# Kernel tuning notes

Measured on AMD Instinct MI355X. Metric: run time of the kernel, lower is better.

The kernel has to match this reference:

```python
import jax, jax.numpy as jnp
import numpy as np

B, U, D, N, O = 128, 16, 256, 1024, 256
RES_CONN, IN_CONN, BIAS_P = 0.2, 0.2, 0.5


def _fixed_bernoulli(rng, heads, rows, cols, conn):
    # each column has exactly nb = int(conn*rows) ones (as in the torch code)
    nb = max(1, int(conn * rows))
    r = rng.random((heads, rows, cols))
    thr = np.sort(r, axis=1)[:, nb - 1:nb, :]
    return (r <= thr).astype(np.float32)


def setup_inputs() -> dict:
    rng = np.random.default_rng(0)
    # recurrent weights: normal * fixed-bernoulli mask, normalized by spectral radius
    W = rng.normal(size=(U, N, N)).astype(np.float32) * _fixed_bernoulli(rng, U, N, N, RES_CONN)
    sr0 = np.abs(np.linalg.eigvals(W.astype(np.float64))).max(axis=-1).astype(np.float32).reshape(U, 1, 1)
    W = W / sr0
    Win = _fixed_bernoulli(rng, U, D, N, IN_CONN)
    bias = (rng.random((U, 1, N)) < BIAS_P).astype(np.float32)
    Wout = rng.normal(size=(U, N, O)).astype(np.float32)
    adaptive_lr = rng.random((U, D, 1)).astype(np.float32)
    sr = rng.random((U, 1, 1)).astype(np.float32)
    temperature = np.ones((1,), np.float32)
    X = rng.normal(size=(B, U, D)).astype(np.float32)
    state = rng.normal(size=(B, U, N)).astype(np.float32)
    arrs = dict(X=X, state=state, W=W, Win=Win, bias=bias, Wout=Wout,
                sr=sr, adaptive_lr=adaptive_lr, temperature=temperature)
    return {k: jnp.asarray(v) for k, v in arrs.items()}


def reference(X, state, W, Win, bias, Wout, sr, adaptive_lr, temperature):
    # X: [B,U,D] -> [B,U,1,D]; state: [B,U,N] -> [B,U,1,N]
    x = X[:, :, None, :]
    s = state[:, :, None, :]
    # adaptive per-unit learning rate: softmax over the units axis
    lr = jax.nn.softmax(jnp.einsum('buid,udk->buik', x, adaptive_lr) / temperature, axis=1)  # [B,U,1,1]
    feed = jnp.einsum('buid,udn->buin', x, Win)            # [B,U,1,N]
    echo = jnp.einsum('buin,unm->buim', s, W * sr) + bias  # [B,U,1,N]
    new_state = (1.0 - lr) * s + lr * jnp.tanh(feed + echo)
    output = jnp.einsum('buin,uno->buio', new_state, Wout)  # [B,U,1,O]
    return new_state[:, :, 0, :], output[:, :, 0, :]
```

## Files before the change

### kernel.cpp

```cpp
#include <hip/hip_runtime.h>
#include <math.h>

#define Bsz 128
#define Usz 16
#define Dsz 256
#define Nsz 1024
#define Osz 256
#define BK  64
#define LDT 72

typedef __attribute__((ext_vector_type(2))) unsigned int u32x2;
typedef __attribute__((ext_vector_type(4))) unsigned int u32x4;
typedef __attribute__((ext_vector_type(4))) float f32x4;
typedef __attribute__((ext_vector_type(8))) short bf16x8;

__device__ __forceinline__ unsigned int fbits(float f) {
    union { float f; unsigned int u; } v; v.f = f; return v.u;
}
__device__ __forceinline__ unsigned int pk(float lo, float hi) {
    return __builtin_amdgcn_perm(fbits(hi), fbits(lo), 0x07060302u);
}
__device__ __forceinline__ unsigned short bf16t(float f) {
    return (unsigned short)(fbits(f) >> 16);
}

__device__ __forceinline__ void sync_nodrain() {
    __builtin_amdgcn_sched_barrier(0);
    asm volatile("s_waitcnt lgkmcnt(0)");
    __builtin_amdgcn_sched_barrier(0);
    __builtin_amdgcn_s_barrier();
    __builtin_amdgcn_sched_barrier(0);
}

__global__ __launch_bounds__(256)
void lr_kernel(const float* __restrict__ X, const float* __restrict__ alr,
               const float* __restrict__ temp, float* __restrict__ lr)
{
    const int b = blockIdx.x;
    const int t = threadIdx.x;
    const int u = t >> 4;
    const int l = t & 15;
    const f32x4* xp = (const f32x4*)(X + ((size_t)b * Usz + u) * Dsz + l * 16);
    const f32x4* ap = (const f32x4*)(alr + (size_t)u * Dsz + l * 16);
    float s = 0.f;
    #pragma unroll
    for (int j = 0; j < 4; j++) {
        const f32x4 xv = xp[j], av = ap[j];
        s += xv[0]*av[0] + xv[1]*av[1] + xv[2]*av[2] + xv[3]*av[3];
    }
    s += __shfl_down(s, 8, 16);
    s += __shfl_down(s, 4, 16);
    s += __shfl_down(s, 2, 16);
    s += __shfl_down(s, 1, 16);
    __shared__ float logits[16];
    if (l == 0) logits[u] = s;
    __syncthreads();
    if (t < 16) {
        const float T = temp[0];
        float m = -1e30f;
        #pragma unroll
        for (int i = 0; i < 16; i++) m = fmaxf(m, logits[i] / T);
        float sum = 0.f;
        #pragma unroll
        for (int i = 0; i < 16; i++) sum += expf(logits[i] / T - m);
        lr[(size_t)b * Usz + t] = expf(logits[t] / T - m) / sum;
    }
}

__global__ __launch_bounds__(512)
void state_gemm(const float* __restrict__ X, const float* __restrict__ state,
                const float* __restrict__ W, const float* __restrict__ Win,
                const float* __restrict__ bias, const float* __restrict__ sr,
                const float* __restrict__ lr, float* __restrict__ out0)
{
    const int id = blockIdx.x;
    const int u  = id & 15;
    const int nt = id >> 4;

    const int tid  = threadIdx.x;
    const int wave = tid >> 6;
    const int lane = tid & 63;
    const int l16  = lane & 15, kgl = lane >> 4;
    const int wm = wave & 3, wn = wave >> 2;

    __shared__ unsigned short As[2][128 * LDT];
    __shared__ unsigned short Bs[2][32 * LDT];

    const float sru = sr[u];
    const int col0 = nt * 32;

    const int rA = tid >> 2;
    const int cA = (tid & 3) * 16;
    const int kB = tid >> 3;
    const int nB = (tid & 7) * 4;
    const int gB = kB >> 3, kL = kB & 7;

    f32x4 rAE[4], rAO[4];
    f32x4 rBE,    rBO;

    auto ldA = [&](int s, f32x4 (&ra)[4]) {
        const int k0 = s * BK;
        const float* base = (k0 < Dsz)
            ? X     + ((size_t)rA * Usz + u) * Dsz + k0 + cA
            : state + ((size_t)rA * Usz + u) * Nsz + (k0 - Dsz) + cA;
        #pragma unroll
        for (int j = 0; j < 4; j++) ra[j] = *(const f32x4*)(base + 4 * j);
    };
    auto ldB = [&](int s, f32x4& rb) {
        const int k0 = s * BK;
        const float* base = (k0 < Dsz)
            ? Win + (size_t)u * Dsz * Nsz + (size_t)(k0 + kB) * Nsz + col0 + nB
            : W   + (size_t)u * Nsz * Nsz + (size_t)(k0 - Dsz + kB) * Nsz + col0 + nB;
        rb = *(const f32x4*)base;
    };
    auto wrA = [&](int p, f32x4 (&ra)[4]) {
        u32x4 w0, w1;
        w0[0] = pk(ra[0][0], ra[0][1]); w0[1] = pk(ra[0][2], ra[0][3]);
        w0[2] = pk(ra[1][0], ra[1][1]); w0[3] = pk(ra[1][2], ra[1][3]);
        w1[0] = pk(ra[2][0], ra[2][1]); w1[1] = pk(ra[2][2], ra[2][3]);
        w1[2] = pk(ra[3][0], ra[3][1]); w1[3] = pk(ra[3][2], ra[3][3]);
        *(u32x4*)&As[p][rA * LDT + cA]     = w0;
        *(u32x4*)&As[p][rA * LDT + cA + 8] = w1;
    };
    auto wrB = [&](int p, f32x4& rb, float sc) {
        const int c = tid & 7;
        const int go = ((gB ^ c) << 3) + kL;
        #pragma unroll
        for (int e = 0; e < 4; e++)
            Bs[p][(nB + e) * LDT + go] = bf16t(rb[e] * sc);
    };
    auto rdB = [&](int p, int kk) -> bf16x8 {
        const int n = wn * 16 + l16;
        const int go = (((kk * 4 + kgl) ^ (n >> 2)) << 3);
        return *(const bf16x8*)&Bs[p][n * LDT + go];
    };

    f32x4 acc[2] = {};
    auto comp = [&](int p) {
        #pragma unroll
        for (int kk = 0; kk < 2; kk++) {
            const bf16x8 bf = rdB(p, kk);
            #pragma unroll
            for (int mi = 0; mi < 2; mi++) {
                const bf16x8 af = *(const bf16x8*)&As[p][(wm * 32 + mi * 16 + l16) * LDT + kk * 32 + kgl * 8];
                acc[mi] = __builtin_amdgcn_mfma_f32_16x16x32_bf16(af, bf, acc[mi], 0, 0, 0);
            }
        }
    };
    auto scB = [&](int s) -> float { return (s * BK < Dsz) ? 1.f : sru; };

    ldA(0, rAE); ldB(0, rBE);
    ldA(1, rAO); ldB(1, rBO);
    wrA(0, rAE); wrB(0, rBE, scB(0));
    sync_nodrain();

    for (int s2 = 0; s2 < 10; s2++) {
        const int s = 2 * s2;
        if (s + 2 < 20) { ldA(s + 2, rAE); ldB(s + 2, rBE); }
        wrA(1, rAO); wrB(1, rBO, scB(s + 1));
        comp(0);
        sync_nodrain();
        if (s + 3 < 20) { ldA(s + 3, rAO); ldB(s + 3, rBO); }
        if (s + 2 < 20) { wrA(0, rAE); wrB(0, rBE, scB(s + 2)); }
        comp(1);
        sync_nodrain();
    }

    const int gcol = col0 + wn * 16 + l16;
    const float bi = bias[u * Nsz + gcol];
    #pragma unroll
    for (int mi = 0; mi < 2; mi++) {
        #pragma unroll
        for (int rg = 0; rg < 4; rg++) {
            const int grow = wm * 32 + mi * 16 + kgl * 4 + rg;
            const size_t idx = ((size_t)grow * Usz + u) * Nsz + gcol;
            const float th = tanhf(acc[mi][rg] + bi);
            const float lv = lr[grow * Usz + u];
            out0[idx] = (1.f - lv) * state[idx] + lv * th;
        }
    }
}

__global__ __launch_bounds__(512)
void out_gemm(const float* __restrict__ ns, const float* __restrict__ Wout,
              float* __restrict__ dst, int nsteps, int partial)
{
    const int id = blockIdx.x;
    const int ot = id & 7;
    const int u  = (id >> 3) & 15;
    const int ks = id >> 7;
    const int kbase = ks * nsteps * BK;

    const int tid  = threadIdx.x;
    const int wave = tid >> 6;
    const int lane = tid & 63;
    const int l16  = lane & 15, kgl = lane >> 4;
    const int wm = wave & 3, wn = wave >> 2;

    __shared__ unsigned short As[2][128 * LDT];
    __shared__ unsigned short Bs[2][32 * LDT];

    const int col0 = ot * 32;
    const int rA = tid >> 2;
    const int cA = (tid & 3) * 16;
    const int kB = tid >> 3;
    const int nB = (tid & 7) * 4;
    const int gB = kB >> 3, kL = kB & 7;

    f32x4 rAE[4], rAO[4];
    f32x4 rBE,    rBO;

    auto ldA = [&](int s, f32x4 (&ra)[4]) {
        const float* base = ns + ((size_t)rA * Usz + u) * Nsz + kbase + s * BK + cA;
        #pragma unroll
        for (int j = 0; j < 4; j++) ra[j] = *(const f32x4*)(base + 4 * j);
    };
    auto ldB = [&](int s, f32x4& rb) {
        rb = *(const f32x4*)(Wout + (size_t)u * Nsz * Osz
                             + (size_t)(kbase + s * BK + kB) * Osz + col0 + nB);
    };
    auto wrA = [&](int p, f32x4 (&ra)[4]) {
        u32x4 w0, w1;
        w0[0] = pk(ra[0][0], ra[0][1]); w0[1] = pk(ra[0][2], ra[0][3]);
        w0[2] = pk(ra[1][0], ra[1][1]); w0[3] = pk(ra[1][2], ra[1][3]);
        w1[0] = pk(ra[2][0], ra[2][1]); w1[1] = pk(ra[2][2], ra[2][3]);
        w1[2] = pk(ra[3][0], ra[3][1]); w1[3] = pk(ra[3][2], ra[3][3]);
        *(u32x4*)&As[p][rA * LDT + cA]     = w0;
        *(u32x4*)&As[p][rA * LDT + cA + 8] = w1;
    };
    auto wrB = [&](int p, f32x4& rb) {
        const int c = tid & 7;
        const int go = ((gB ^ c) << 3) + kL;
        #pragma unroll
        for (int e = 0; e < 4; e++)
            Bs[p][(nB + e) * LDT + go] = bf16t(rb[e]);
    };
    auto rdB = [&](int p, int kk) -> bf16x8 {
        const int n = wn * 16 + l16;
        const int go = (((kk * 4 + kgl) ^ (n >> 2)) << 3);
        return *(const bf16x8*)&Bs[p][n * LDT + go];
    };

    f32x4 acc[2] = {};
    auto comp = [&](int p) {
        #pragma unroll
        for (int kk = 0; kk < 2; kk++) {
            const bf16x8 bf = rdB(p, kk);
            #pragma unroll
            for (int mi = 0; mi < 2; mi++) {
                const bf16x8 af = *(const bf16x8*)&As[p][(wm * 32 + mi * 16 + l16) * LDT + kk * 32 + kgl * 8];
                acc[mi] = __builtin_amdgcn_mfma_f32_16x16x32_bf16(af, bf, acc[mi], 0, 0, 0);
            }
        }
    };

    ldA(0, rAE); ldB(0, rBE);
    ldA(1, rAO); ldB(1, rBO);
    wrA(0, rAE); wrB(0, rBE);
    sync_nodrain();

    for (int s2 = 0; s2 < nsteps / 2; s2++) {
        const int s = 2 * s2;
        if (s + 2 < nsteps) { ldA(s + 2, rAE); ldB(s + 2, rBE); }
        wrA(1, rAO); wrB(1, rBO);
        comp(0);
        sync_nodrain();
        if (s + 3 < nsteps) { ldA(s + 3, rAO); ldB(s + 3, rBO); }
        if (s + 2 < nsteps) { wrA(0, rAE); wrB(0, rBE); }
        comp(1);
        sync_nodrain();
    }

    const int gcol = col0 + wn * 16 + l16;
    #pragma unroll
    for (int mi = 0; mi < 2; mi++) {
        #pragma unroll
        for (int rg = 0; rg < 4; rg++) {
            const int grow = wm * 32 + mi * 16 + kgl * 4 + rg;
            if (partial)
                dst[(((size_t)ks * 16 + u) * 128 + grow) * 256 + gcol] = acc[mi][rg];
            else
                dst[((size_t)grow * Usz + u) * Osz + gcol] = acc[mi][rg];
        }
    }
}

__global__ __launch_bounds__(256)
void out_reduce(const float* __restrict__ part, float* __restrict__ out1)
{
    const size_t i = (size_t)blockIdx.x * 256 + threadIdx.x;
    const size_t base = i * 4;
    const int m = (int)(base >> 12);
    const int u = (int)((base >> 8) & 15);
    const int o = (int)(base & 255);

    const size_t pb = ((size_t)u * 128 + m) * 256 + o;
    const size_t slab = (size_t)16 * 128 * 256;
    f32x4 s = *(const f32x4*)(part + pb);
    s += *(const f32x4*)(part + pb + slab);
    s += *(const f32x4*)(part + pb + 2 * slab);
    s += *(const f32x4*)(part + pb + 3 * slab);
    *(f32x4*)(out1 + base) = s;
}

extern "C" void kernel_launch(void* const* d_in, const int* in_sizes, int n_in,
                              void* d_out, int out_size, void* d_ws, size_t ws_size,
                              hipStream_t stream)
{
    (void)in_sizes; (void)n_in; (void)out_size;
    const float* X     = (const float*)d_in[0];
    const float* state = (const float*)d_in[1];
    const float* W     = (const float*)d_in[2];
    const float* Win   = (const float*)d_in[3];
    const float* bias  = (const float*)d_in[4];
    const float* Wout  = (const float*)d_in[5];
    const float* sr    = (const float*)d_in[6];
    const float* alr   = (const float*)d_in[7];
    const float* temp  = (const float*)d_in[8];

    float* out0 = (float*)d_out;
    float* out1 = out0 + (size_t)Bsz * Usz * Nsz;
    float* lr   = (float*)d_ws;

    const size_t p_off   = 8192;
    const size_t p_bytes = (size_t)4 * 16 * 128 * 256 * 4;

    lr_kernel<<<Bsz, 256, 0, stream>>>(X, alr, temp, lr);
    state_gemm<<<512, 512, 0, stream>>>(X, state, W, Win, bias, sr, lr, out0);

    if (ws_size >= p_off + p_bytes) {
        float* part = (float*)((char*)d_ws + p_off);
        out_gemm<<<512, 512, 0, stream>>>(out0, Wout, part, 4, 1);
        out_reduce<<<512, 256, 0, stream>>>(part, out1);
    } else {
        out_gemm<<<128, 512, 0, stream>>>(out0, Wout, out1, 16, 0);
    }
}
```

Measured before the change: 185.5 us.

## Pre-pack operands to bf16 MFMA fragment layout and run register-only GEMMs

Adds packing kernels that convert W·sr, Win, Wout, X/state and the new state into bf16 tiles already laid out as MFMA fragments. New GEMM kernels then load these fragments straight into registers with a 3-stage register prefetch and skip the LDS staging. The point is to remove shared-memory traffic, barriers and per-tile conversion from the GEMMs. In exchange it adds several extra launches and a full rewrite of the weights every call, about 40 MB of bf16 written and read again, and it only runs when the workspace is large enough.

```diff
diff --git a/kernel.cpp b/kernel.cpp
--- a/kernel.cpp
+++ b/kernel.cpp
@@ -67,11 +67,222 @@
     }
 }
 
+
+__global__ __launch_bounds__(256)
+void pack_A(const float* __restrict__ X, const float* __restrict__ state,
+            unsigned short* __restrict__ Abf)
+{
+    const int t = blockIdx.x * 256 + threadIdx.x;
+    const int kq = t % 160;
+    const int mu = t / 160;
+    const int u = mu & 15, m = mu >> 4;
+    const float* sp = (kq < 32)
+        ? X     + (size_t)mu * Dsz + kq * 8
+        : state + (size_t)mu * Nsz + (kq - 32) * 8;
+    const f32x4 v0 = *(const f32x4*)sp;
+    const f32x4 v1 = *(const f32x4*)(sp + 4);
+    u32x4 w;
+    w[0]=pk(v0[0],v0[1]); w[1]=pk(v0[2],v0[3]); w[2]=pk(v1[0],v1[1]); w[3]=pk(v1[2],v1[3]);
+    *(u32x4*)(Abf + (size_t)(u*8 + (m>>4))*20480 + (kq>>2)*512 + (kq&3)*128 + (m&15)*8) = w;
+}
+
+__global__ __launch_bounds__(256)
+void pack_ns(const float* __restrict__ ns, unsigned short* __restrict__ NsP)
+{
+    const int t = blockIdx.x * 256 + threadIdx.x;
+    const int kq = t & 127;
+    const int mu = t >> 7;
+    const int u = mu & 15, m = mu >> 4;
+    const float* sp = ns + (size_t)mu * Nsz + kq * 8;
+    const f32x4 v0 = *(const f32x4*)sp;
+    const f32x4 v1 = *(const f32x4*)(sp + 4);
+    u32x4 w;
+    w[0]=pk(v0[0],v0[1]); w[1]=pk(v0[2],v0[3]); w[2]=pk(v1[0],v1[1]); w[3]=pk(v1[2],v1[3]);
+    *(u32x4*)(NsP + (size_t)(u*8 + (m>>4))*16384 + (kq>>2)*512 + (kq&3)*128 + (m&15)*8) = w;
+}
+
+__global__ __launch_bounds__(256)
+void prep_w(const float* __restrict__ srcA, const float* __restrict__ srcB,
+            const float* __restrict__ scale, unsigned short* __restrict__ dst,
+            int KA, int Ktot, int N, int S, int Tn)
+{
+    const int nblkN = N >> 6;
+    const int per_u = (Ktot >> 6) * nblkN;
+    const int bid = blockIdx.x;
+    const int u   = bid / per_u;
+    const int rem = bid % per_u;
+    const int kt  = rem / nblkN;
+    const int nt4 = rem % nblkN;
+
+    const int t  = threadIdx.x;
+    const int kr = t >> 4;
+    const int nc = (t & 15) * 4;
+    const int n0 = nt4 * 64;
+
+    const float sc = scale ? scale[u] : 1.f;
+
+    __shared__ float tl[64][68];
+
+    #pragma unroll
+    for (int r = 0; r < 4; r++) {
+        const int kl = kr + r * 16;
+        const int k  = kt * 64 + kl;
+        const float* sp = (k < KA)
+            ? srcA + ((size_t)u * KA + k) * N + n0 + nc
+            : srcB + ((size_t)u * (Ktot - KA) + (k - KA)) * N + n0 + nc;
+        f32x4 v = *(const f32x4*)sp;
+        if (k >= KA) v *= sc;
+        *(f32x4*)&tl[kl][nc] = v;
+    }
+    __syncthreads();
+    #pragma unroll
+    for (int fi = 0; fi < 2; fi++) {
+        const int f   = t + fi * 256;
+        const int l   = f & 15;
+        const int g   = (f >> 4) & 7;
+        const int ntl = f >> 7;
+        float x[8];
+        #pragma unroll
+        for (int i = 0; i < 8; i++) x[i] = tl[g*8 + i][ntl*16 + l];
+        u32x4 w;
+        w[0]=pk(x[0],x[1]); w[1]=pk(x[2],x[3]); w[2]=pk(x[4],x[5]); w[3]=pk(x[6],x[7]);
+        const int tn = nt4*4 + ntl;
+        const int s  = kt*2 + (g>>2);
+        *(u32x4*)(dst + ((size_t)(u*Tn + tn)*S + s)*512 + (g&3)*128 + l*8) = w;
+    }
+}
+
+__global__ __launch_bounds__(512, 4)
+void state_gemm_reg(const float* __restrict__ state,
+                    const unsigned short* __restrict__ Abf,
+                    const unsigned short* __restrict__ Bp,
+                    const float* __restrict__ bias, const float* __restrict__ lr,
+                    float* __restrict__ out0)
+{
+    const int id  = blockIdx.x;
+    const int u   = id & 15;
+    const int nt2 = id >> 4;
+
+    const int tid = threadIdx.x;
+    const int wave = tid >> 6, lane = tid & 63;
+    const int l16 = lane & 15, kgl = lane >> 4;
+    const int wm = wave & 3, wn = wave >> 2;
+    const int mt0 = wm * 2;
+    const int tn  = nt2 * 2 + wn;
+
+    const unsigned short* pa0 = Abf + (size_t)(u*8 + mt0)    *20480 + kgl*128 + l16*8;
+    const unsigned short* pa1 = Abf + (size_t)(u*8 + mt0 + 1)*20480 + kgl*128 + l16*8;
+    const unsigned short* pb  = Bp  + (size_t)(u*64 + tn)    *20480 + kgl*128 + l16*8;
+
+    bf16x8 a0[3], a1[3], bb[3];
+    f32x4 acc0 = {}, acc1 = {};
+
+    a0[0] = *(const bf16x8*)(pa0);        a1[0] = *(const bf16x8*)(pa1);        bb[0] = *(const bf16x8*)(pb);
+    a0[1] = *(const bf16x8*)(pa0 + 512);  a1[1] = *(const bf16x8*)(pa1 + 512);  bb[1] = *(const bf16x8*)(pb + 512);
+
+    #pragma unroll
+    for (int s = 0; s < 40; s++) {
+        const int st = s % 3, nx = (s + 2) % 3;
+        if (s + 2 < 40) {
+            a0[nx] = *(const bf16x8*)(pa0 + (size_t)(s + 2) * 512);
+            a1[nx] = *(const bf16x8*)(pa1 + (size_t)(s + 2) * 512);
+            bb[nx] = *(const bf16x8*)(pb  + (size_t)(s + 2) * 512);
+        }
+        acc0 = __builtin_amdgcn_mfma_f32_16x16x32_bf16(a0[st], bb[st], acc0, 0, 0, 0);
+        acc1 = __builtin_amdgcn_mfma_f32_16x16x32_bf16(a1[st], bb[st], acc1, 0, 0, 0);
+    }
+
+    const int gcol = tn * 16 + l16;
+    const float bi = bias[u * Nsz + gcol];
+    #pragma unroll
+    for (int mi = 0; mi < 2; mi++) {
+        const f32x4 a = mi ? acc1 : acc0;
+        #pragma unroll
+        for (int rg = 0; rg < 4; rg++) {
+            const int grow = (mt0 + mi) * 16 + kgl * 4 + rg;
+            const size_t idx = ((size_t)grow * Usz + u) * Nsz + gcol;
+            const float th = tanhf(a[rg] + bi);
+            const float lv = lr[grow * Usz + u];
+            out0[idx] = (1.f - lv) * state[idx] + lv * th;
+        }
+    }
+}
+
+__global__ __launch_bounds__(512, 4)
+void out_gemm_reg(const unsigned short* __restrict__ NsP,
+                  const unsigned short* __restrict__ Wp,
+                  float* __restrict__ part)
+{
+    const int id = blockIdx.x;
+    const int ot = id & 7;
+    const int u  = (id >> 3) & 15;
+    const int ks = id >> 7;
+    const int sb = ks * 8;
+
+    const int tid = threadIdx.x;
+    const int wave = tid >> 6, lane = tid & 63;
+    const int l16 = lane & 15, kgl = lane >> 4;
+    const int wm = wave & 3, wn = wave >> 2;
+    const int mt0 = wm * 2;
+    const int tn  = ot * 2 + wn;
+
+    const unsigned short* pa0 = NsP + (size_t)(u*8 + mt0)    *16384 + (size_t)sb*512 + kgl*128 + l16*8;
+    const unsigned short* pa1 = NsP + (size_t)(u*8 + mt0 + 1)*16384 + (size_t)sb*512 + kgl*128 + l16*8;
+    const unsigned short* pb  = Wp  + (size_t)(u*16 + tn)    *16384 + (size_t)sb*512 + kgl*128 + l16*8;
+
+    bf16x8 a0[3], a1[3], bb[3];
+    f32x4 acc0 = {}, acc1 = {};
+
+    a0[0] = *(const bf16x8*)(pa0);        a1[0] = *(const bf16x8*)(pa1);        bb[0] = *(const bf16x8*)(pb);
+    a0[1] = *(const bf16x8*)(pa0 + 512);  a1[1] = *(const bf16x8*)(pa1 + 512);  bb[1] = *(const bf16x8*)(pb + 512);
+
+    #pragma unroll
+    for (int s = 0; s < 8; s++) {
+        const int st = s % 3, nx = (s + 2) % 3;
+        if (s + 2 < 8) {
+            a0[nx] = *(const bf16x8*)(pa0 + (size_t)(s + 2) * 512);
+            a1[nx] = *(const bf16x8*)(pa1 + (size_t)(s + 2) * 512);
+            bb[nx] = *(const bf16x8*)(pb  + (size_t)(s + 2) * 512);
+        }
+        acc0 = __builtin_amdgcn_mfma_f32_16x16x32_bf16(a0[st], bb[st], acc0, 0, 0, 0);
+        acc1 = __builtin_amdgcn_mfma_f32_16x16x32_bf16(a1[st], bb[st], acc1, 0, 0, 0);
+    }
+
+    const int gcol = tn * 16 + l16;
+    #pragma unroll
+    for (int mi = 0; mi < 2; mi++) {
+        const f32x4 a = mi ? acc1 : acc0;
+        #pragma unroll
+        for (int rg = 0; rg < 4; rg++) {
+            const int grow = (mt0 + mi) * 16 + kgl * 4 + rg;
+            part[(((size_t)ks * 16 + u) * 128 + grow) * 256 + gcol] = a[rg];
+        }
+    }
+}
+
+__global__ __launch_bounds__(256)
+void out_reduce(const float* __restrict__ part, float* __restrict__ out1)
+{
+    const size_t i = (size_t)blockIdx.x * 256 + threadIdx.x;
+    const size_t base = i * 4;
+    const int m = (int)(base >> 12);
+    const int u = (int)((base >> 8) & 15);
+    const int o = (int)(base & 255);
+
+    const size_t pb = ((size_t)u * 128 + m) * 256 + o;
+    const size_t slab = (size_t)16 * 128 * 256;
+    f32x4 s = *(const f32x4*)(part + pb);
+    s += *(const f32x4*)(part + pb + slab);
+    s += *(const f32x4*)(part + pb + 2 * slab);
+    s += *(const f32x4*)(part + pb + 3 * slab);
+    *(f32x4*)(out1 + base) = s;
+}
+
 __global__ __launch_bounds__(512)
-void state_gemm(const float* __restrict__ X, const float* __restrict__ state,
-                const float* __restrict__ W, const float* __restrict__ Win,
-                const float* __restrict__ bias, const float* __restrict__ sr,
-                const float* __restrict__ lr, float* __restrict__ out0)
+void state_gemm_fb(const float* __restrict__ X, const float* __restrict__ state,
+                   const float* __restrict__ W, const float* __restrict__ Win,
+                   const float* __restrict__ bias, const float* __restrict__ sr,
+                   const float* __restrict__ lr, float* __restrict__ out0)
 {
     const int id = blockIdx.x;
     const int u  = id & 15;
@@ -182,8 +393,8 @@
 }
 
 __global__ __launch_bounds__(512)
-void out_gemm(const float* __restrict__ ns, const float* __restrict__ Wout,
-              float* __restrict__ dst, int nsteps, int partial)
+void out_gemm_fb(const float* __restrict__ ns, const float* __restrict__ Wout,
+                 float* __restrict__ dst, int nsteps, int partial)
 {
     const int id = blockIdx.x;
     const int ot = id & 7;
@@ -285,24 +496,6 @@
     }
 }
 
-__global__ __launch_bounds__(256)
-void out_reduce(const float* __restrict__ part, float* __restrict__ out1)
-{
-    const size_t i = (size_t)blockIdx.x * 256 + threadIdx.x;
-    const size_t base = i * 4;
-    const int m = (int)(base >> 12);
-    const int u = (int)((base >> 8) & 15);
-    const int o = (int)(base & 255);
-
-    const size_t pb = ((size_t)u * 128 + m) * 256 + o;
-    const size_t slab = (size_t)16 * 128 * 256;
-    f32x4 s = *(const f32x4*)(part + pb);
-    s += *(const f32x4*)(part + pb + slab);
-    s += *(const f32x4*)(part + pb + 2 * slab);
-    s += *(const f32x4*)(part + pb + 3 * slab);
-    *(f32x4*)(out1 + base) = s;
-}
-
 extern "C" void kernel_launch(void* const* d_in, const int* in_sizes, int n_in,
                               void* d_out, int out_size, void* d_ws, size_t ws_size,
                               hipStream_t stream)
@@ -322,17 +515,41 @@
     float* out1 = out0 + (size_t)Bsz * Usz * Nsz;
     float* lr   = (float*)d_ws;
 
-    const size_t p_off   = 8192;
-    const size_t p_bytes = (size_t)4 * 16 * 128 * 256 * 4;
+    const size_t p_off    = 8192;
+    const size_t p_bytes  = (size_t)4 * 16 * 128 * 256 * 4;
+    const size_t bp_off   = p_off + p_bytes;
+    const size_t bp_bytes = (size_t)16 * 1280 * 1024 * 2;
+    const size_t wo_off   = bp_off + bp_bytes;
+    const size_t wo_bytes = (size_t)16 * 1024 * 256 * 2;
+    const size_t ab_off   = wo_off + wo_bytes;
+    const size_t ab_bytes = (size_t)128 * 16 * 1280 * 2;
+    const size_t ns_off   = ab_off + ab_bytes;
+    const size_t ns_bytes = (size_t)128 * 16 * 1024 * 2;
+    const size_t need     = ns_off + ns_bytes;
 
     lr_kernel<<<Bsz, 256, 0, stream>>>(X, alr, temp, lr);
-    state_gemm<<<512, 512, 0, stream>>>(X, state, W, Win, bias, sr, lr, out0);
-
-    if (ws_size >= p_off + p_bytes) {
+
+    if (ws_size >= need) {
+        float*          part = (float*)((char*)d_ws + p_off);
+        unsigned short* Bp   = (unsigned short*)((char*)d_ws + bp_off);
+        unsigned short* Wp   = (unsigned short*)((char*)d_ws + wo_off);
+        unsigned short* Abf  = (unsigned short*)((char*)d_ws + ab_off);
+        unsigned short* NsP  = (unsigned short*)((char*)d_ws + ns_off);
+
+        prep_w<<<5120, 256, 0, stream>>>(Win, W, sr, Bp, Dsz, 1280, Nsz, 40, 64);
+        prep_w<<<1024, 256, 0, stream>>>(Wout, Wout, nullptr, Wp, Nsz, Nsz, Osz, 32, 16);
+        pack_A<<<1280, 256, 0, stream>>>(X, state, Abf);
+        state_gemm_reg<<<512, 512, 0, stream>>>(state, Abf, Bp, bias, lr, out0);
+        pack_ns<<<1024, 256, 0, stream>>>(out0, NsP);
+        out_gemm_reg<<<512, 512, 0, stream>>>(NsP, Wp, part);
+        out_reduce<<<512, 256, 0, stream>>>(part, out1);
+    } else if (ws_size >= p_off + p_bytes) {
         float* part = (float*)((char*)d_ws + p_off);
-        out_gemm<<<512, 512, 0, stream>>>(out0, Wout, part, 4, 1);
+        state_gemm_fb<<<512, 512, 0, stream>>>(X, state, W, Win, bias, sr, lr, out0);
+        out_gemm_fb<<<512, 512, 0, stream>>>(out0, Wout, part, 4, 1);
         out_reduce<<<512, 256, 0, stream>>>(part, out1);
     } else {
-        out_gemm<<<128, 512, 0, stream>>>(out0, Wout, out1, 16, 0);
-    }
-}
+        state_gemm_fb<<<512, 512, 0, stream>>>(X, state, W, Win, bias, sr, lr, out0);
+        out_gemm_fb<<<128, 512, 0, stream>>>(out0, Wout, out1, 16, 0);
+    }
+}
```

Result: slower. 204.0 us (+9.9%).

## Split-K the state GEMM into two halves with a separate tanh epilogue kernel

Applied to the files above, without the earlier changes.

The state GEMM (K=1280, from X plus state) is split into two K halves of 640. That doubles the grid to 1024 blocks for better occupancy on the many CUs. Partial sums go to workspace, and a new elementwise kernel reduces them and applies bias, tanh and the lr blend. The split kernel also switches its A tile in LDS to an XOR-swizzled unpadded layout instead of padded rows. The cost is extra global traffic for the partials (16 MB written then read) and one more kernel launch.

```diff
diff --git a/kernel.cpp b/kernel.cpp
--- a/kernel.cpp
+++ b/kernel.cpp
@@ -67,15 +67,16 @@
     }
 }
 
-__global__ __launch_bounds__(512)
-void state_gemm(const float* __restrict__ X, const float* __restrict__ state,
-                const float* __restrict__ W, const float* __restrict__ Win,
-                const float* __restrict__ bias, const float* __restrict__ sr,
-                const float* __restrict__ lr, float* __restrict__ out0)
+__global__ __launch_bounds__(512, 8)
+void state_gemm_sk(const float* __restrict__ X, const float* __restrict__ state,
+                   const float* __restrict__ W, const float* __restrict__ Win,
+                   const float* __restrict__ sr, float* __restrict__ part2)
 {
     const int id = blockIdx.x;
     const int u  = id & 15;
-    const int nt = id >> 4;
+    const int nt = (id >> 4) & 31;
+    const int ks = id >> 9;
+    const int kbase = ks * 640;
 
     const int tid  = threadIdx.x;
     const int wave = tid >> 6;
@@ -83,12 +84,148 @@
     const int l16  = lane & 15, kgl = lane >> 4;
     const int wm = wave & 3, wn = wave >> 2;
 
+    __shared__ unsigned short As[2][128 * 64];
+    __shared__ unsigned short Bs[2][32 * 64];
+
+    const float sru = sr[u];
+    const int col0 = nt * 32;
+
+    const int rA = tid >> 2;
+    const int cA = (tid & 3) * 16;
+    const int g0 = (tid & 3) * 2;
+    const int sw = rA & 7;
+    const int kB = tid >> 3;
+    const int nB = (tid & 7) * 4;
+    const int gB = kB >> 3, kL = kB & 7;
+
+    f32x4 rAE[4], rAO[4];
+    f32x4 rBE,    rBO;
+
+    auto ldA = [&](int s, f32x4 (&ra)[4]) {
+        const int k0 = kbase + s * BK;
+        const float* base = (k0 < Dsz)
+            ? X     + ((size_t)rA * Usz + u) * Dsz + k0 + cA
+            : state + ((size_t)rA * Usz + u) * Nsz + (k0 - Dsz) + cA;
+        #pragma unroll
+        for (int j = 0; j < 4; j++) ra[j] = *(const f32x4*)(base + 4 * j);
+    };
+    auto ldB = [&](int s, f32x4& rb) {
+        const int k0 = kbase + s * BK;
+        const float* base = (k0 < Dsz)
+            ? Win + (size_t)u * Dsz * Nsz + (size_t)(k0 + kB) * Nsz + col0 + nB
+            : W   + (size_t)u * Nsz * Nsz + (size_t)(k0 - Dsz + kB) * Nsz + col0 + nB;
+        rb = *(const f32x4*)base;
+    };
+    auto wrA = [&](int p, f32x4 (&ra)[4]) {
+        u32x4 w0, w1;
+        w0[0] = pk(ra[0][0], ra[0][1]); w0[1] = pk(ra[0][2], ra[0][3]);
+        w0[2] = pk(ra[1][0], ra[1][1]); w0[3] = pk(ra[1][2], ra[1][3]);
+        w1[0] = pk(ra[2][0], ra[2][1]); w1[1] = pk(ra[2][2], ra[2][3]);
+        w1[2] = pk(ra[3][0], ra[3][1]); w1[3] = pk(ra[3][2], ra[3][3]);
+        *(u32x4*)&As[p][rA * 64 + ((g0       ^ sw) << 3)] = w0;
+        *(u32x4*)&As[p][rA * 64 + (((g0 | 1) ^ sw) << 3)] = w1;
+    };
+    auto wrB = [&](int p, f32x4& rb, float sc) {
+        const int c = tid & 7;
+        const int go = ((gB ^ c) << 3) + kL;
+        #pragma unroll
+        for (int e = 0; e < 4; e++)
+            Bs[p][(nB + e) * 64 + go] = bf16t(rb[e] * sc);
+    };
+    auto rdB = [&](int p, int kk) -> bf16x8 {
+        const int n = wn * 16 + l16;
+        const int go = (((kk * 4 + kgl) ^ (n >> 2)) << 3);
+        return *(const bf16x8*)&Bs[p][n * 64 + go];
+    };
+
+    f32x4 acc[2] = {};
+    auto comp = [&](int p) {
+        #pragma unroll
+        for (int kk = 0; kk < 2; kk++) {
+            const bf16x8 bf = rdB(p, kk);
+            #pragma unroll
+            for (int mi = 0; mi < 2; mi++) {
+                const int r = wm * 32 + mi * 16 + l16;
+                const bf16x8 af = *(const bf16x8*)&As[p][r * 64 + (((kk * 4 + kgl) ^ (r & 7)) << 3)];
+                acc[mi] = __builtin_amdgcn_mfma_f32_16x16x32_bf16(af, bf, acc[mi], 0, 0, 0);
+            }
+        }
+    };
+    auto scB = [&](int s) -> float { return (kbase + s * BK < Dsz) ? 1.f : sru; };
+
+    ldA(0, rAE); ldB(0, rBE);
+    ldA(1, rAO); ldB(1, rBO);
+    wrA(0, rAE); wrB(0, rBE, scB(0));
+    sync_nodrain();
+
+    for (int s2 = 0; s2 < 5; s2++) {
+        const int s = 2 * s2;
+        if (s + 2 < 10) { ldA(s + 2, rAE); ldB(s + 2, rBE); }
+        wrA(1, rAO); wrB(1, rBO, scB(s + 1));
+        comp(0);
+        sync_nodrain();
+        if (s + 3 < 10) { ldA(s + 3, rAO); ldB(s + 3, rBO); }
+        if (s + 2 < 10) { wrA(0, rAE); wrB(0, rBE, scB(s + 2)); }
+        comp(1);
+        sync_nodrain();
+    }
+
+    const int gcol = col0 + wn * 16 + l16;
+    float* dst = part2 + (size_t)ks * 128 * Usz * Nsz;
+    #pragma unroll
+    for (int mi = 0; mi < 2; mi++) {
+        #pragma unroll
+        for (int rg = 0; rg < 4; rg++) {
+            const int grow = wm * 32 + mi * 16 + kgl * 4 + rg;
+            dst[((size_t)grow * Usz + u) * Nsz + gcol] = acc[mi][rg];
+        }
+    }
+}
+
+__global__ __launch_bounds__(256)
+void state_ep(const float* __restrict__ part2, const float* __restrict__ state,
+              const float* __restrict__ bias, const float* __restrict__ lr,
+              float* __restrict__ out0)
+{
+    const size_t i = (size_t)blockIdx.x * 256 + threadIdx.x;
+    const size_t base = i * 4;
+    const int m = (int)(i >> 12);
+    const int u = (int)((i >> 8) & 15);
+    const int n = (int)((i & 255) * 4);
+
+    const size_t slab = (size_t)128 * Usz * Nsz;
+    f32x4 s = *(const f32x4*)(part2 + base);
+    s += *(const f32x4*)(part2 + base + slab);
+    const f32x4 bi = *(const f32x4*)(bias + u * Nsz + n);
+    const f32x4 st = *(const f32x4*)(state + base);
+    const float lv = lr[m * Usz + u];
+    f32x4 o;
+    #pragma unroll
+    for (int e = 0; e < 4; e++)
+        o[e] = (1.f - lv) * st[e] + lv * tanhf(s[e] + bi[e]);
+    *(f32x4*)(out0 + base) = o;
+}
+
+__global__ __launch_bounds__(512)
+void out_gemm_fb(const float* __restrict__ ns, const float* __restrict__ Wout,
+                 float* __restrict__ dst, int nsteps, int partial)
+{
+    const int id = blockIdx.x;
+    const int ot = id & 7;
+    const int u  = (id >> 3) & 15;
+    const int ks = id >> 7;
+    const int kbase = ks * nsteps * BK;
+
+    const int tid  = threadIdx.x;
+    const int wave = tid >> 6;
+    const int lane = tid & 63;
+    const int l16  = lane & 15, kgl = lane >> 4;
+    const int wm = wave & 3, wn = wave >> 2;
+
     __shared__ unsigned short As[2][128 * LDT];
     __shared__ unsigned short Bs[2][32 * LDT];
 
-    const float sru = sr[u];
-    const int col0 = nt * 32;
-
+    const int col0 = ot * 32;
     const int rA = tid >> 2;
     const int cA = (tid & 3) * 16;
     const int kB = tid >> 3;
@@ -99,19 +236,13 @@
     f32x4 rBE,    rBO;
 
     auto ldA = [&](int s, f32x4 (&ra)[4]) {
-        const int k0 = s * BK;
-        const float* base = (k0 < Dsz)
-            ? X     + ((size_t)rA * Usz + u) * Dsz + k0 + cA
-            : state + ((size_t)rA * Usz + u) * Nsz + (k0 - Dsz) + cA;
+        const float* base = ns + ((size_t)rA * Usz + u) * Nsz + kbase + s * BK + cA;
         #pragma unroll
         for (int j = 0; j < 4; j++) ra[j] = *(const f32x4*)(base + 4 * j);
     };
     auto ldB = [&](int s, f32x4& rb) {
-        const int k0 = s * BK;
-        const float* base = (k0 < Dsz)
-            ? Win + (size_t)u * Dsz * Nsz + (size_t)(k0 + kB) * Nsz + col0 + nB
-            : W   + (size_t)u * Nsz * Nsz + (size_t)(k0 - Dsz + kB) * Nsz + col0 + nB;
-        rb = *(const f32x4*)base;
+        rb = *(const f32x4*)(Wout + (size_t)u * Nsz * Osz
+                             + (size_t)(kbase + s * BK + kB) * Osz + col0 + nB);
     };
     auto wrA = [&](int p, f32x4 (&ra)[4]) {
         u32x4 w0, w1;
@@ -122,12 +253,12 @@
         *(u32x4*)&As[p][rA * LDT + cA]     = w0;
         *(u32x4*)&As[p][rA * LDT + cA + 8] = w1;
     };
-    auto wrB = [&](int p, f32x4& rb, float sc) {
+    auto wrB = [&](int p, f32x4& rb) {
         const int c = tid & 7;
         const int go = ((gB ^ c) << 3) + kL;
         #pragma unroll
         for (int e = 0; e < 4; e++)
-            Bs[p][(nB + e) * LDT + go] = bf16t(rb[e] * sc);
+            Bs[p][(nB + e) * LDT + go] = bf16t(rb[e]);
     };
     auto rdB = [&](int p, int kk) -> bf16x8 {
         const int n = wn * 16 + l16;
@@ -147,49 +278,65 @@
             }
         }
     };
-    auto scB = [&](int s) -> float { return (s * BK < Dsz) ? 1.f : sru; };
 
     ldA(0, rAE); ldB(0, rBE);
     ldA(1, rAO); ldB(1, rBO);
-    wrA(0, rAE); wrB(0, rBE, scB(0));
+    wrA(0, rAE); wrB(0, rBE);
     sync_nodrain();
 
-    for (int s2 = 0; s2 < 10; s2++) {
+    for (int s2 = 0; s2 < nsteps / 2; s2++) {
         const int s = 2 * s2;
-        if (s + 2 < 20) { ldA(s + 2, rAE); ldB(s + 2, rBE); }
-        wrA(1, rAO); wrB(1, rBO, scB(s + 1));
+        if (s + 2 < nsteps) { ldA(s + 2, rAE); ldB(s + 2, rBE); }
+        wrA(1, rAO); wrB(1, rBO);
         comp(0);
         sync_nodrain();
-        if (s + 3 < 20) { ldA(s + 3, rAO); ldB(s + 3, rBO); }
-        if (s + 2 < 20) { wrA(0, rAE); wrB(0, rBE, scB(s + 2)); }
+        if (s + 3 < nsteps) { ldA(s + 3, rAO); ldB(s + 3, rBO); }
+        if (s + 2 < nsteps) { wrA(0, rAE); wrB(0, rBE); }
         comp(1);
         sync_nodrain();
     }
 
     const int gcol = col0 + wn * 16 + l16;
-    const float bi = bias[u * Nsz + gcol];
     #pragma unroll
     for (int mi = 0; mi < 2; mi++) {
         #pragma unroll
         for (int rg = 0; rg < 4; rg++) {
             const int grow = wm * 32 + mi * 16 + kgl * 4 + rg;
-            const size_t idx = ((size_t)grow * Usz + u) * Nsz + gcol;
-            const float th = tanhf(acc[mi][rg] + bi);
-            const float lv = lr[grow * Usz + u];
-            out0[idx] = (1.f - lv) * state[idx] + lv * th;
-        }
-    }
+            if (partial)
+                dst[(((size_t)ks * 16 + u) * 128 + grow) * 256 + gcol] = acc[mi][rg];
+            else
+                dst[((size_t)grow * Usz + u) * Osz + gcol] = acc[mi][rg];
+        }
+    }
+}
+
+__global__ __launch_bounds__(256)
+void out_reduce(const float* __restrict__ part, float* __restrict__ out1)
+{
+    const size_t i = (size_t)blockIdx.x * 256 + threadIdx.x;
+    const size_t base = i * 4;
+    const int m = (int)(base >> 12);
+    const int u = (int)((base >> 8) & 15);
+    const int o = (int)(base & 255);
+
+    const size_t pb = ((size_t)u * 128 + m) * 256 + o;
+    const size_t slab = (size_t)16 * 128 * 256;
+    f32x4 s = *(const f32x4*)(part + pb);
+    s += *(const f32x4*)(part + pb + slab);
+    s += *(const f32x4*)(part + pb + 2 * slab);
+    s += *(const f32x4*)(part + pb + 3 * slab);
+    *(f32x4*)(out1 + base) = s;
 }
 
 __global__ __launch_bounds__(512)
-void out_gemm(const float* __restrict__ ns, const float* __restrict__ Wout,
-              float* __restrict__ dst, int nsteps, int partial)
+void state_gemm_fb(const float* __restrict__ X, const float* __restrict__ state,
+                   const float* __restrict__ W, const float* __restrict__ Win,
+                   const float* __restrict__ bias, const float* __restrict__ sr,
+                   const float* __restrict__ lr, float* __restrict__ out0)
 {
     const int id = blockIdx.x;
-    const int ot = id & 7;
-    const int u  = (id >> 3) & 15;
-    const int ks = id >> 7;
-    const int kbase = ks * nsteps * BK;
+    const int u  = id & 15;
+    const int nt = id >> 4;
 
     const int tid  = threadIdx.x;
     const int wave = tid >> 6;
@@ -200,7 +347,9 @@
     __shared__ unsigned short As[2][128 * LDT];
     __shared__ unsigned short Bs[2][32 * LDT];
 
-    const int col0 = ot * 32;
+    const float sru = sr[u];
+    const int col0 = nt * 32;
+
     const int rA = tid >> 2;
     const int cA = (tid & 3) * 16;
     const int kB = tid >> 3;
@@ -211,13 +360,19 @@
     f32x4 rBE,    rBO;
 
     auto ldA = [&](int s, f32x4 (&ra)[4]) {
-        const float* base = ns + ((size_t)rA * Usz + u) * Nsz + kbase + s * BK + cA;
+        const int k0 = s * BK;
+        const float* base = (k0 < Dsz)
+            ? X     + ((size_t)rA * Usz + u) * Dsz + k0 + cA
+            : state + ((size_t)rA * Usz + u) * Nsz + (k0 - Dsz) + cA;
         #pragma unroll
         for (int j = 0; j < 4; j++) ra[j] = *(const f32x4*)(base + 4 * j);
     };
     auto ldB = [&](int s, f32x4& rb) {
-        rb = *(const f32x4*)(Wout + (size_t)u * Nsz * Osz
-                             + (size_t)(kbase + s * BK + kB) * Osz + col0 + nB);
+        const int k0 = s * BK;
+        const float* base = (k0 < Dsz)
+            ? Win + (size_t)u * Dsz * Nsz + (size_t)(k0 + kB) * Nsz + col0 + nB
+            : W   + (size_t)u * Nsz * Nsz + (size_t)(k0 - Dsz + kB) * Nsz + col0 + nB;
+        rb = *(const f32x4*)base;
     };
     auto wrA = [&](int p, f32x4 (&ra)[4]) {
         u32x4 w0, w1;
@@ -228,12 +383,12 @@
         *(u32x4*)&As[p][rA * LDT + cA]     = w0;
         *(u32x4*)&As[p][rA * LDT + cA + 8] = w1;
     };
-    auto wrB = [&](int p, f32x4& rb) {
+    auto wrB = [&](int p, f32x4& rb, float sc) {
         const int c = tid & 7;
         const int go = ((gB ^ c) << 3) + kL;
         #pragma unroll
         for (int e = 0; e < 4; e++)
-            Bs[p][(nB + e) * LDT + go] = bf16t(rb[e]);
+            Bs[p][(nB + e) * LDT + go] = bf16t(rb[e] * sc);
     };
     auto rdB = [&](int p, int kk) -> bf16x8 {
         const int n = wn * 16 + l16;
@@ -253,54 +408,38 @@
             }
         }
     };
+    auto scB = [&](int s) -> float { return (s * BK < Dsz) ? 1.f : sru; };
 
     ldA(0, rAE); ldB(0, rBE);
     ldA(1, rAO); ldB(1, rBO);
-    wrA(0, rAE); wrB(0, rBE);
+    wrA(0, rAE); wrB(0, rBE, scB(0));
     sync_nodrain();
 
-    for (int s2 = 0; s2 < nsteps / 2; s2++) {
+    for (int s2 = 0; s2 < 10; s2++) {
         const int s = 2 * s2;
-        if (s + 2 < nsteps) { ldA(s + 2, rAE); ldB(s + 2, rBE); }
-        wrA(1, rAO); wrB(1, rBO);
+        if (s + 2 < 20) { ldA(s + 2, rAE); ldB(s + 2, rBE); }
+        wrA(1, rAO); wrB(1, rBO, scB(s + 1));
         comp(0);
         sync_nodrain();
-        if (s + 3 < nsteps) { ldA(s + 3, rAO); ldB(s + 3, rBO); }
-        if (s + 2 < nsteps) { wrA(0, rAE); wrB(0, rBE); }
+        if (s + 3 < 20) { ldA(s + 3, rAO); ldB(s + 3, rBO); }
+        if (s + 2 < 20) { wrA(0, rAE); wrB(0, rBE, scB(s + 2)); }
         comp(1);
         sync_nodrain();
     }
 
     const int gcol = col0 + wn * 16 + l16;
+    const float bi = bias[u * Nsz + gcol];
     #pragma unroll
     for (int mi = 0; mi < 2; mi++) {
         #pragma unroll
         for (int rg = 0; rg < 4; rg++) {
             const int grow = wm * 32 + mi * 16 + kgl * 4 + rg;
-            if (partial)
-                dst[(((size_t)ks * 16 + u) * 128 + grow) * 256 + gcol] = acc[mi][rg];
-            else
-                dst[((size_t)grow * Usz + u) * Osz + gcol] = acc[mi][rg];
-        }
-    }
-}
-
-__global__ __launch_bounds__(256)
-void out_reduce(const float* __restrict__ part, float* __restrict__ out1)
-{
-    const size_t i = (size_t)blockIdx.x * 256 + threadIdx.x;
-    const size_t base = i * 4;
-    const int m = (int)(base >> 12);
-    const int u = (int)((base >> 8) & 15);
-    const int o = (int)(base & 255);
-
-    const size_t pb = ((size_t)u * 128 + m) * 256 + o;
-    const size_t slab = (size_t)16 * 128 * 256;
-    f32x4 s = *(const f32x4*)(part + pb);
-    s += *(const f32x4*)(part + pb + slab);
-    s += *(const f32x4*)(part + pb + 2 * slab);
-    s += *(const f32x4*)(part + pb + 3 * slab);
-    *(f32x4*)(out1 + base) = s;
+            const size_t idx = ((size_t)grow * Usz + u) * Nsz + gcol;
+            const float th = tanhf(acc[mi][rg] + bi);
+            const float lv = lr[grow * Usz + u];
+            out0[idx] = (1.f - lv) * state[idx] + lv * th;
+        }
+    }
 }
 
 extern "C" void kernel_launch(void* const* d_in, const int* in_sizes, int n_in,
@@ -322,17 +461,28 @@
     float* out1 = out0 + (size_t)Bsz * Usz * Nsz;
     float* lr   = (float*)d_ws;
 
-    const size_t p_off   = 8192;
-    const size_t p_bytes = (size_t)4 * 16 * 128 * 256 * 4;
+    const size_t p_off    = 8192;
+    const size_t p_bytes  = (size_t)4 * 16 * 128 * 256 * 4;
+    const size_t p2_off   = p_off + p_bytes;
+    const size_t p2_bytes = (size_t)2 * 128 * 16 * 1024 * 4;
+    const size_t need     = p2_off + p2_bytes;
 
     lr_kernel<<<Bsz, 256, 0, stream>>>(X, alr, temp, lr);
-    state_gemm<<<512, 512, 0, stream>>>(X, state, W, Win, bias, sr, lr, out0);
-
-    if (ws_size >= p_off + p_bytes) {
+
+    if (ws_size >= need) {
+        float* part  = (float*)((char*)d_ws + p_off);
+        float* part2 = (float*)((char*)d_ws + p2_off);
+        state_gemm_sk<<<1024, 512, 0, stream>>>(X, state, W, Win, sr, part2);
+        state_ep<<<2048, 256, 0, stream>>>(part2, state, bias, lr, out0);
+        out_gemm_fb<<<512, 512, 0, stream>>>(out0, Wout, part, 4, 1);
+        out_reduce<<<512, 256, 0, stream>>>(part, out1);
+    } else if (ws_size >= p_off + p_bytes) {
         float* part = (float*)((char*)d_ws + p_off);
-        out_gemm<<<512, 512, 0, stream>>>(out0, Wout, part, 4, 1);
+        state_gemm_fb<<<512, 512, 0, stream>>>(X, state, W, Win, bias, sr, lr, out0);
+        out_gemm_fb<<<512, 512, 0, stream>>>(out0, Wout, part, 4, 1);
         out_reduce<<<512, 256, 0, stream>>>(part, out1);
     } else {
-        out_gemm<<<128, 512, 0, stream>>>(out0, Wout, out1, 16, 0);
-    }
-}
+        state_gemm_fb<<<512, 512, 0, stream>>>(X, state, W, Win, bias, sr, lr, out0);
+        out_gemm_fb<<<128, 512, 0, stream>>>(out0, Wout, out1, 16, 0);
+    }
+}
```

Result: slower. 200.1 us (+7.9%).
